# Performance work log

Hardware: AMD Instinct MI355X
Metric: run time of the kernel (lower is better)

## Reference

```python
import jax, jax.numpy as jnp
import numpy as np
from jax import lax

FH, FW, STRIDE = 100, 160, 16
IMG_H, IMG_W = FH * STRIDE, FW * STRIDE
A = 9
PRE_NMS, POST_NMS = 6000, 300  # prediction-path caps (training=0)
IOU_THR = 0.7
NEG = jnp.float32(-1e9)


def _make_anchor_map():
    # classic 3 scales x 3 aspect ratios, stride-16 grid, (y1,x1,y2,x2)
    scales = np.array([128.0, 256.0, 512.0], np.float32)
    ratios = np.array([0.5, 1.0, 2.0], np.float32)
    hs = (scales[:, None] * np.sqrt(ratios)[None, :]).reshape(-1)  # [9]
    ws = (scales[:, None] / np.sqrt(ratios)[None, :]).reshape(-1)
    cy = ((np.arange(FH, dtype=np.float32) + 0.5) * STRIDE)[:, None, None]
    cx = ((np.arange(FW, dtype=np.float32) + 0.5) * STRIDE)[None, :, None]
    y1 = np.broadcast_to(cy - 0.5 * hs, (FH, FW, A))
    x1 = np.broadcast_to(cx - 0.5 * ws, (FH, FW, A))
    y2 = np.broadcast_to(cy + 0.5 * hs, (FH, FW, A))
    x2 = np.broadcast_to(cx + 0.5 * ws, (FH, FW, A))
    am = np.stack([y1, x1, y2, x2], axis=-1)  # [FH,FW,9,4]
    return jnp.asarray(am.reshape(1, FH, FW, A * 4))


def setup_inputs() -> dict:
    key = jax.random.key(0)
    ks = jax.random.split(key, 6)
    return {
        "input_image": jax.random.uniform(ks[0], (1, IMG_H, IMG_W, 3), jnp.float32),
        "feature_map": jax.random.normal(ks[1], (1, FH, FW, 512), jnp.float32),
        "anchor_map": _make_anchor_map(),
        "anchor_valid_map": jnp.ones((1, FH, FW, A), jnp.float32),
        "W1": 0.01 * jax.random.normal(ks[2], (3, 3, 512, 512), jnp.float32),
        "b1": jnp.zeros((512,), jnp.float32),
        "Wc": 0.01 * jax.random.normal(ks[3], (1, 1, 512, A), jnp.float32),
        "bc": jnp.zeros((A,), jnp.float32),
        "Wr": 0.01 * jax.random.normal(ks[4], (1, 1, 512, 4 * A), jnp.float32),
        "br": jnp.zeros((4 * A,), jnp.float32),
        "training": 0,
    }


def _conv(x, w, b):
    return lax.conv_general_dilated(
        x, w, (1, 1), "SAME", dimension_numbers=("NHWC", "HWIO", "NHWC")
    ) + b


def _iou_one_vs_all(box, boxes):
    yy1 = jnp.maximum(box[0], boxes[:, 0])
    xx1 = jnp.maximum(box[1], boxes[:, 1])
    yy2 = jnp.minimum(box[2], boxes[:, 2])
    xx2 = jnp.minimum(box[3], boxes[:, 3])
    inter = jnp.maximum(yy2 - yy1, 0.0) * jnp.maximum(xx2 - xx1, 0.0)
    a1 = jnp.maximum(box[2] - box[0], 0.0) * jnp.maximum(box[3] - box[1], 0.0)
    a2 = jnp.maximum(boxes[:, 2] - boxes[:, 0], 0.0) * jnp.maximum(boxes[:, 3] - boxes[:, 1], 0.0)
    return inter / (a1 + a2 - inter + 1e-8)


def _nms(boxes, scores, max_out, iou_thr):
    # greedy NMS with fixed iteration count (padded with zero boxes)
    def step(s, _):
        i = jnp.argmax(s)
        best = s[i]
        box = boxes[i]
        valid = best > NEG * 0.5
        ious = _iou_one_vs_all(box, boxes)
        s = jnp.where(ious > iou_thr, NEG, s)
        s = s.at[i].set(NEG)
        out = jnp.where(valid, box, jnp.zeros_like(box))
        return s, out

    _, sel = lax.scan(step, scores, None, length=max_out)
    return sel  # [max_out, 4]


def reference(input_image, feature_map, anchor_map, anchor_valid_map,
              W1, b1, Wc, bc, Wr, br, training):
    pre_nms = 12000 if training else PRE_NMS
    post_nms = 2000 if training else POST_NMS
    # RPN head convs
    y = jax.nn.relu(_conv(feature_map, W1, b1))
    scores_map = jax.nn.sigmoid(_conv(y, Wc, bc))          # [1,FH,FW,9]
    reg_map = _conv(y, Wr, br)                              # [1,FH,FW,36]
    # flatten (extract_valid)
    anchors = anchor_map.reshape(-1, 4)                     # [N,4] (y1,x1,y2,x2)
    obj = scores_map.reshape(-1)                            # [N]
    deltas = reg_map.reshape(-1, 4)                         # [N,4] (ty,tx,th,tw)
    # delta -> bbox decode (means=0, stds=1)
    ah = anchors[:, 2] - anchors[:, 0]
    aw = anchors[:, 3] - anchors[:, 1]
    acy = anchors[:, 0] + 0.5 * ah
    acx = anchors[:, 1] + 0.5 * aw
    cy = acy + deltas[:, 0] * ah
    cx = acx + deltas[:, 1] * aw
    h = ah * jnp.exp(deltas[:, 2])
    w = aw * jnp.exp(deltas[:, 3])
    props = jnp.stack([cy - 0.5 * h, cx - 0.5 * w, cy + 0.5 * h, cx + 0.5 * w], axis=1)
    # sort desc by score, keep top pre_nms
    sc, idx = lax.top_k(obj, pre_nms)
    props = props[idx]
    # clip to image
    img_h = jnp.float32(input_image.shape[1])
    img_w = jnp.float32(input_image.shape[2])
    tl = jnp.maximum(props[:, 0:2], 0.0)
    y2 = jnp.minimum(props[:, 2], img_h)[:, None]
    x2 = jnp.minimum(props[:, 3], img_w)[:, None]
    props = jnp.concatenate([tl, y2, x2], axis=1)
    # min-size filter (>=16 on each side), via score masking (jit-safe)
    hh = props[:, 2] - props[:, 0]
    ww = props[:, 3] - props[:, 1]
    sc = jnp.where((hh >= 16.0) & (ww >= 16.0), sc, NEG)
    proposals = _nms(props, sc, post_nms, IOU_THR)          # [post_nms,4], zero-padded
    return scores_map, reg_map, proposals
```

## Files before the change

kernel.cpp:

```cpp
#include <hip/hip_runtime.h>
#include <math.h>

#define FHh 100
#define FWw 160
#define CIN 512
#define COUT 512
#define NPIX 16000
#define NANCH 144000
#define PRE_NMS 6000
#define POST_NMS 300
#define EQCAP 8192

#define BM 128
#define BN 128
#define BK 16
#define AST 130

typedef double d4 __attribute__((ext_vector_type(4)));

__device__ __forceinline__ unsigned fkey(float x){
  unsigned b = __float_as_uint(x);
  return (b & 0x80000000u) ? ~b : (b | 0x80000000u);
}
__device__ __forceinline__ unsigned long long dkey(double x){
  unsigned long long u = (unsigned long long)__double_as_longlong(x);
  return (u & 0x8000000000000000ull) ? ~u : (u | 0x8000000000000000ull);
}
__device__ __forceinline__ unsigned long long shfl_u64(unsigned long long x, int lane){
  unsigned lo = (unsigned)x, hi = (unsigned)(x >> 32);
  lo = __shfl(lo, lane, 64);
  hi = __shfl(hi, lane, 64);
  return ((unsigned long long)hi << 32) | lo;
}

__global__ __launch_bounds__(256) void prep_all(
    const float* __restrict__ fm, const float* __restrict__ Wc, const float* __restrict__ Wr,
    double* __restrict__ fmd, double* __restrict__ WcT, double* __restrict__ WrT)
{
  const int bid = blockIdx.x;
  if (bid < 8000){
    const int i = bid*256 + threadIdx.x;
    const float4 v = ((const float4*)fm)[i];
    double2* d = (double2*)(fmd + (size_t)i*4);
    d[0] = make_double2((double)v.x, (double)v.y);
    d[1] = make_double2((double)v.z, (double)v.w);
  } else {
    const int gid = (bid - 8000)*256 + threadIdx.x;
    if (gid < 45*512){
      const int n = gid >> 9, ci = gid & 511;
      if (n < 9) WcT[(size_t)n*512 + ci] = (double)Wc[ci*9 + n];
      else       WrT[(size_t)(n-9)*512 + ci] = (double)Wr[ci*36 + (n-9)];
    }
  }
}

__global__ __launch_bounds__(256, 2) void conv_gemm(
    const double* __restrict__ fmd, const float* __restrict__ W1,
    const float* __restrict__ b1, double* __restrict__ yd)
{
  __shared__ double As[BK * AST];
  __shared__ double Bs[BK * BN];
  const int bid  = blockIdx.x;
  const int cg   = bid / 125;
  const int tile = bid - cg*125;
  const int rp   = tile / 5;
  const int xseg = tile - rp*5;
  const int x0   = xseg*32;
  const int row0 = rp*4;
  const int co0  = cg*128;

  const int tid = threadIdx.x;
  const int lane = tid & 63;
  const int kl = lane >> 4;
  const int cl = lane & 15;
  const int wv = tid >> 6;
  const int wr = wv >> 1;
  const int wc = wv & 1;

  const int aoffA = kl*AST + wr*64 + cl;
  const int aoffB = kl*BN + wc*64 + cl;

  const int apx = tid >> 2;
  const int aks = (tid & 3) * 4;
  const int prA = apx >> 5;
  const int ac  = apx & 31;
  const int bkrow = tid >> 7;
  const int bcl   = tid & 127;

  d4 acc[4][4];
  #pragma unroll
  for (int mt = 0; mt < 4; ++mt)
    #pragma unroll
    for (int nt = 0; nt < 4; ++nt) acc[mt][nt] = (d4){0.0, 0.0, 0.0, 0.0};

  double pA0, pA1, pA2, pA3;
  double pB0, pB1, pB2, pB3;
  float pw[8];

  {
    const int grA = row0 + prA - 1;
    const int grB = grA + 2;
    const int gx  = x0 + ac - 1;
    if (grA >= 0 && gx >= 0){
      const double* p = fmd + ((size_t)(grA*FWw + gx))*CIN + aks;
      pA0 = p[0]; pA1 = p[1]; pA2 = p[2]; pA3 = p[3];
    } else { pA0 = pA1 = pA2 = pA3 = 0.0; }
    if (gx >= 0){
      const double* p = fmd + ((size_t)(grB*FWw + gx))*CIN + aks;
      pB0 = p[0]; pB1 = p[1]; pB2 = p[2]; pB3 = p[3];
    } else { pB0 = pB1 = pB2 = pB3 = 0.0; }
    const float* wb = W1 + (size_t)co0 + bcl;
    #pragma unroll
    for (int s = 0; s < 8; ++s) pw[s] = wb[(size_t)(2*s + bkrow)*512];
  }

  for (int ch = 0; ch < 288; ++ch){
    __syncthreads();
    As[(aks+0)*AST + apx] = pA0;
    As[(aks+1)*AST + apx] = pA1;
    As[(aks+2)*AST + apx] = pA2;
    As[(aks+3)*AST + apx] = pA3;
    As[(aks+0)*AST + apx + 64] = pB0;
    As[(aks+1)*AST + apx + 64] = pB1;
    As[(aks+2)*AST + apx + 64] = pB2;
    As[(aks+3)*AST + apx + 64] = pB3;
    #pragma unroll
    for (int s = 0; s < 8; ++s) Bs[s*256 + tid] = (double)pw[s];
    __syncthreads();
    const int nc = ch + 1;
    if (nc < 288){
      const int tap = nc >> 5;
      const int k0  = (nc & 31) * BK;
      const int dy = tap/3 - 1, dx = tap%3 - 1;
      const int grA = row0 + prA + dy;
      const int grB = grA + 2;
      const int gx  = x0 + ac + dx;
      const bool gxok = (gx >= 0 && gx < FWw);
      if (gxok && grA >= 0 && grA < FHh){
        const double* p = fmd + ((size_t)(grA*FWw + gx))*CIN + k0 + aks;
        pA0 = p[0]; pA1 = p[1]; pA2 = p[2]; pA3 = p[3];
      } else { pA0 = pA1 = pA2 = pA3 = 0.0; }
      if (gxok && grB >= 0 && grB < FHh){
        const double* p = fmd + ((size_t)(grB*FWw + gx))*CIN + k0 + aks;
        pB0 = p[0]; pB1 = p[1]; pB2 = p[2]; pB3 = p[3];
      } else { pB0 = pB1 = pB2 = pB3 = 0.0; }
      const float* wb = W1 + ((size_t)(tap*512 + k0 + bkrow))*512 + co0 + bcl;
      #pragma unroll
      for (int s = 0; s < 8; ++s) pw[s] = wb[(size_t)(2*s)*512];
    }
    #pragma unroll
    for (int k4 = 0; k4 < 4; ++k4){
      const double* Ap = As + k4*4*AST + aoffA;
      const double* Bp = Bs + k4*4*BN + aoffB;
      const double a0 = Ap[0], a1 = Ap[16], a2 = Ap[32], a3 = Ap[48];
      const double b0 = Bp[0], b1v = Bp[16], b2 = Bp[32], b3 = Bp[48];
      acc[0][0] = __builtin_amdgcn_mfma_f64_16x16x4f64(a0, b0,  acc[0][0], 0, 0, 0);
      acc[0][1] = __builtin_amdgcn_mfma_f64_16x16x4f64(a0, b1v, acc[0][1], 0, 0, 0);
      acc[0][2] = __builtin_amdgcn_mfma_f64_16x16x4f64(a0, b2,  acc[0][2], 0, 0, 0);
      acc[0][3] = __builtin_amdgcn_mfma_f64_16x16x4f64(a0, b3,  acc[0][3], 0, 0, 0);
      acc[1][0] = __builtin_amdgcn_mfma_f64_16x16x4f64(a1, b0,  acc[1][0], 0, 0, 0);
      acc[1][1] = __builtin_amdgcn_mfma_f64_16x16x4f64(a1, b1v, acc[1][1], 0, 0, 0);
      acc[1][2] = __builtin_amdgcn_mfma_f64_16x16x4f64(a1, b2,  acc[1][2], 0, 0, 0);
      acc[1][3] = __builtin_amdgcn_mfma_f64_16x16x4f64(a1, b3,  acc[1][3], 0, 0, 0);
      acc[2][0] = __builtin_amdgcn_mfma_f64_16x16x4f64(a2, b0,  acc[2][0], 0, 0, 0);
      acc[2][1] = __builtin_amdgcn_mfma_f64_16x16x4f64(a2, b1v, acc[2][1], 0, 0, 0);
      acc[2][2] = __builtin_amdgcn_mfma_f64_16x16x4f64(a2, b2,  acc[2][2], 0, 0, 0);
      acc[2][3] = __builtin_amdgcn_mfma_f64_16x16x4f64(a2, b3,  acc[2][3], 0, 0, 0);
      acc[3][0] = __builtin_amdgcn_mfma_f64_16x16x4f64(a3, b0,  acc[3][0], 0, 0, 0);
      acc[3][1] = __builtin_amdgcn_mfma_f64_16x16x4f64(a3, b1v, acc[3][1], 0, 0, 0);
      acc[3][2] = __builtin_amdgcn_mfma_f64_16x16x4f64(a3, b2,  acc[3][2], 0, 0, 0);
      acc[3][3] = __builtin_amdgcn_mfma_f64_16x16x4f64(a3, b3,  acc[3][3], 0, 0, 0);
    }
  }
  double bb[4];
  #pragma unroll
  for (int nt = 0; nt < 4; ++nt) bb[nt] = (double)b1[co0 + wc*64 + nt*16 + cl];
  #pragma unroll
  for (int mt = 0; mt < 4; ++mt){
    #pragma unroll
    for (int i = 0; i < 4; ++i){
      const int pxl = wr*64 + mt*16 + 4*i + kl;
      const int gpx = (row0 + (pxl >> 5))*FWw + x0 + (pxl & 31);
      double* yrow = yd + (size_t)gpx*CIN + co0 + wc*64 + cl;
      #pragma unroll
      for (int nt = 0; nt < 4; ++nt){
        yrow[nt*16] = fmax(acc[mt][nt][i] + bb[nt], 0.0);
      }
    }
  }
}

__global__ __launch_bounds__(256) void head2(
    const double* __restrict__ yd, const double* __restrict__ WcT, const float* __restrict__ bc,
    const double* __restrict__ WrT, const float* __restrict__ br,
    float* __restrict__ out, double* __restrict__ scored, double* __restrict__ regd)
{
  __shared__ double yl[8192];
  const int bid = blockIdx.x, t = threadIdx.x;
  const double2* src = (const double2*)(yd + (size_t)bid * 8192);
  double2* dst = (double2*)yl;
  for (int j = t; j < 4096; j += 256) dst[j] = src[j];
  __syncthreads();
  if (t < 180){
    const int n  = t % 45;
    const int pq = t / 45;
    const double* w = (n < 9) ? (WcT + (size_t)n*512) : (WrT + (size_t)(n-9)*512);
    const double* y0 = yl + (pq*4+0)*512;
    const double* y1 = yl + (pq*4+1)*512;
    const double* y2 = yl + (pq*4+2)*512;
    const double* y3 = yl + (pq*4+3)*512;
    double s0=0.0, s1=0.0, s2=0.0, s3=0.0;
    for (int ci = 0; ci < 512; ++ci){
      const double wv = w[ci];
      s0 = fma(y0[ci], wv, s0);
      s1 = fma(y1[ci], wv, s1);
      s2 = fma(y2[ci], wv, s2);
      s3 = fma(y3[ci], wv, s3);
    }
    const double sv[4] = {s0, s1, s2, s3};
    if (n < 9){
      const double bb = (double)bc[n];
      #pragma unroll
      for (int u = 0; u < 4; ++u){
        const double s = sv[u] + bb;
        const double sig = 1.0 / (1.0 + exp(-s));
        const int gi = (bid*16 + pq*4 + u)*9 + n;
        out[gi] = (float)sig;
        scored[gi] = sig;
      }
    } else {
      const int m = n - 9;
      const double bb = (double)br[m];
      #pragma unroll
      for (int u = 0; u < 4; ++u){
        const double s = sv[u] + bb;
        const int gi = (bid*16 + pq*4 + u)*36 + m;
        out[144000 + gi] = (float)s;
        regd[gi] = s;
      }
    }
  }
}

__global__ __launch_bounds__(256) void decode_hist(
    const float* __restrict__ amap, const double* __restrict__ scored,
    const double* __restrict__ regd, double* __restrict__ boxesd,
    unsigned* __restrict__ key32, unsigned long long* __restrict__ nmskey,
    unsigned* __restrict__ hist)
{
  const int i = blockIdx.x*256 + threadIdx.x;
  if (i >= NANCH) return;
  const double a0=(double)amap[4*i+0], a1=(double)amap[4*i+1];
  const double a2=(double)amap[4*i+2], a3=(double)amap[4*i+3];
  const double d0=regd[4*i+0], d1=regd[4*i+1], d2=regd[4*i+2], d3=regd[4*i+3];
  const double ah = a2 - a0, aw = a3 - a1;
  const double cy = a0 + 0.5*ah + d0*ah;
  const double cx = a1 + 0.5*aw + d1*aw;
  const double h = ah * exp(d2), w = aw * exp(d3);
  double y1 = cy - 0.5*h, x1 = cx - 0.5*w, y2 = cy + 0.5*h, x2 = cx + 0.5*w;
  y1 = fmax(y1, 0.0); x1 = fmax(x1, 0.0);
  y2 = fmin(y2, 1600.0); x2 = fmin(x2, 2560.0);
  boxesd[4*i+0]=y1; boxesd[4*i+1]=x1; boxesd[4*i+2]=y2; boxesd[4*i+3]=x2;
  const double obj = scored[i];
  const bool ok = (y2 - y1 >= 16.0) && (x2 - x1 >= 16.0);
  const unsigned k32 = fkey((float)obj);
  key32[i] = k32;
  nmskey[i] = ok ? dkey(obj) : dkey(-1e9);
  atomicAdd(&hist[k32 >> 16], 1u);
}

__global__ __launch_bounds__(1024) void scan_hi(const unsigned* __restrict__ hist, int* __restrict__ meta){
  __shared__ unsigned part[1024];
  const int t = threadIdx.x;
  unsigned s = 0;
  for (int j = 0; j < 64; ++j) s += hist[65535 - (t*64 + j)];
  part[t] = s;
  __syncthreads();
  for (int off = 1; off < 1024; off <<= 1){
    unsigned v = (t >= off) ? part[t - off] : 0u;
    __syncthreads();
    part[t] += v;
    __syncthreads();
  }
  const unsigned incl = part[t], excl = incl - s;
  if (excl < PRE_NMS && incl >= PRE_NMS){
    unsigned cum = excl;
    for (int j = 0; j < 64; ++j){
      const int bin = 65535 - (t*64 + j);
      const unsigned c = hist[bin];
      if (cum + c >= PRE_NMS){ meta[0] = bin; meta[1] = (int)cum; break; }
      cum += c;
    }
  }
}

__global__ __launch_bounds__(256) void hist_lo(const unsigned* __restrict__ key,
                                               const int* __restrict__ meta, unsigned* __restrict__ hist){
  const int i = blockIdx.x*256 + threadIdx.x;
  if (i < NANCH){
    const unsigned k = key[i];
    if ((int)(k >> 16) == meta[0]) atomicAdd(&hist[k & 0xFFFFu], 1u);
  }
}

__global__ __launch_bounds__(1024) void scan_lo(const unsigned* __restrict__ hist, int* __restrict__ meta){
  __shared__ unsigned part[1024];
  const int t = threadIdx.x;
  const unsigned G0 = (unsigned)meta[1];
  unsigned s = 0;
  for (int j = 0; j < 64; ++j) s += hist[65535 - (t*64 + j)];
  part[t] = s;
  __syncthreads();
  for (int off = 1; off < 1024; off <<= 1){
    unsigned v = (t >= off) ? part[t - off] : 0u;
    __syncthreads();
    part[t] += v;
    __syncthreads();
  }
  const unsigned incl = G0 + part[t], excl = incl - s;
  if (excl < PRE_NMS && incl >= PRE_NMS){
    unsigned cum = excl;
    for (int j = 0; j < 64; ++j){
      const int bin = 65535 - (t*64 + j);
      const unsigned c = hist[bin];
      if (cum + c >= PRE_NMS){
        meta[2] = (int)(((unsigned)meta[0] << 16) | (unsigned)bin);
        meta[3] = (int)cum;
        meta[4] = PRE_NMS - (int)cum;
        break;
      }
      cum += c;
    }
  }
}

__global__ __launch_bounds__(256) void compact_k(
    const unsigned* __restrict__ key, const unsigned long long* __restrict__ nmskey,
    const double* __restrict__ boxesd, const int* __restrict__ meta,
    int* __restrict__ cnt, double* __restrict__ selboxd,
    unsigned long long* __restrict__ selkey, int* __restrict__ eqidx)
{
  const int i = blockIdx.x*256 + threadIdx.x;
  if (i >= NANCH) return;
  const unsigned k = key[i];
  const unsigned T = (unsigned)meta[2];
  if (k > T){
    const int s = atomicAdd(&cnt[0], 1);
    selboxd[4*s+0]=boxesd[4*i+0]; selboxd[4*s+1]=boxesd[4*i+1];
    selboxd[4*s+2]=boxesd[4*i+2]; selboxd[4*s+3]=boxesd[4*i+3];
    selkey[s] = nmskey[i];
  } else if (k == T){
    const int e = atomicAdd(&cnt[1], 1);
    if (e < EQCAP) eqidx[e] = i;
  }
}

__global__ __launch_bounds__(256) void rankeq(
    const double* __restrict__ scored, const double* __restrict__ boxesd,
    const unsigned long long* __restrict__ nmskey,
    const int* __restrict__ meta, const int* __restrict__ cnt,
    const int* __restrict__ eqidx, double* __restrict__ selboxd,
    unsigned long long* __restrict__ selkey)
{
  __shared__ int eq[EQCAP];
  const int t = threadIdx.x;
  int E = cnt[1]; if (E > EQCAP) E = EQCAP;
  const int R = meta[4], G2 = meta[3];
  for (int j = t; j < E; j += 256) eq[j] = eqidx[j];
  __syncthreads();
  for (int j = t; j < E; j += 256){
    const int my = eq[j];
    const double smy = scored[my];
    int rank = 0;
    for (int k2 = 0; k2 < E; ++k2){
      const int ok = eq[k2];
      const double sk = scored[ok];
      rank += ((sk > smy) || (sk == smy && ok < my)) ? 1 : 0;
    }
    if (rank < R){
      const int s = G2 + rank;
      selboxd[4*s+0]=boxesd[4*my+0]; selboxd[4*s+1]=boxesd[4*my+1];
      selboxd[4*s+2]=boxesd[4*my+2]; selboxd[4*s+3]=boxesd[4*my+3];
      selkey[s] = nmskey[my];
    }
  }
}

__global__ __launch_bounds__(256) void rank_scatter(
    const unsigned long long* __restrict__ selkey, const double* __restrict__ selboxd,
    unsigned long long* __restrict__ skeys, double* __restrict__ sboxd)
{
  __shared__ unsigned long long k[PRE_NMS];
  const int t = threadIdx.x;
  for (int j = t; j < PRE_NMS; j += 256) k[j] = selkey[j];
  __syncthreads();
  const int j = blockIdx.x*256 + t;
  if (j >= PRE_NMS) return;
  const unsigned long long kj = k[j];
  int r = 0;
  for (int i = 0; i < PRE_NMS; i += 4){
    r += (int)((k[i+0] > kj) || (k[i+0] == kj && (i+0) < j));
    r += (int)((k[i+1] > kj) || (k[i+1] == kj && (i+1) < j));
    r += (int)((k[i+2] > kj) || (k[i+2] == kj && (i+2) < j));
    r += (int)((k[i+3] > kj) || (k[i+3] == kj && (i+3) < j));
  }
  skeys[r] = kj;
  sboxd[(size_t)r*4+0] = selboxd[(size_t)j*4+0];
  sboxd[(size_t)r*4+1] = selboxd[(size_t)j*4+1];
  sboxd[(size_t)r*4+2] = selboxd[(size_t)j*4+2];
  sboxd[(size_t)r*4+3] = selboxd[(size_t)j*4+3];
}

__global__ __launch_bounds__(256) void iou_bitmap(
    const double* __restrict__ sboxd, unsigned long long* __restrict__ rowbits)
{
  __shared__ double cbx[4096];
  const int g = blockIdx.y;
  const int r0 = blockIdx.x * 16;
  const int t = threadIdx.x;
  const int cbase = g * 1024;
  for (int e = t; e < 4096; e += 256){
    const int bi = cbase + (e >> 2);
    cbx[e] = (bi < PRE_NMS) ? sboxd[(size_t)bi*4 + (e & 3)] : 0.0;
  }
  __syncthreads();
  const int r = r0 + (t >> 4);
  const int w = t & 15;
  const double by1 = sboxd[(size_t)r*4+0], bx1 = sboxd[(size_t)r*4+1];
  const double by2 = sboxd[(size_t)r*4+2], bx2 = sboxd[(size_t)r*4+3];
  const double a1 = fmax(by2-by1, 0.0) * fmax(bx2-bx1, 0.0);
  unsigned long long bits = 0ull;
  for (int b = 0; b < 64; ++b){
    const int bcol = (b + w) & 63;
    const int j = cbase + w*64 + bcol;
    if (j < PRE_NMS){
      const int ce = (w*64 + bcol)*4;
      const double c0 = cbx[ce+0], c1 = cbx[ce+1], c2 = cbx[ce+2], c3 = cbx[ce+3];
      const double yy1 = fmax(by1, c0), xx1 = fmax(bx1, c1);
      const double yy2 = fmin(by2, c2), xx2 = fmin(bx2, c3);
      const double inter = fmax(yy2-yy1, 0.0) * fmax(xx2-xx1, 0.0);
      const double a2 = fmax(c2-c0, 0.0) * fmax(c3-c1, 0.0);
      const double iou = inter / (a1 + a2 - inter + 1e-8);
      if (iou > 0.7) bits |= (1ull << bcol);
    }
  }
  rowbits[(size_t)r*128 + g*16 + w] = bits;
}

__global__ __launch_bounds__(64) void greedy(
    const unsigned long long* __restrict__ skeys, const double* __restrict__ sboxd,
    const unsigned long long* __restrict__ rowbits, float* __restrict__ outp)
{
  const int t = threadIdx.x;
  const unsigned long long KEYTH = dkey(-5.0e8);
  int bad = PRE_NMS;
  for (int j = t; j < PRE_NMS; j += 64){
    if (skeys[j] <= KEYTH){ bad = j; break; }
  }
  #pragma unroll
  for (int off = 32; off > 0; off >>= 1){
    const int o = __shfl_down(bad, off, 64);
    bad = (o < bad) ? o : bad;
  }
  const int ilim = __builtin_amdgcn_readfirstlane(bad);

  unsigned long long s0 = 0ull, s1 = 0ull;
  int emitted = 0;
  for (int i = 0; i < ilim && emitted < POST_NMS; ++i){
    const int w = i >> 6, b = i & 63;
    const unsigned long long w0 = shfl_u64(s0, w & 63);
    const unsigned long long w1 = shfl_u64(s1, (w - 64) & 63);
    const unsigned long long word = (w < 64) ? w0 : w1;
    if (!((word >> b) & 1ull)){
      if (t < 4) outp[4*emitted + t] = (float)sboxd[(size_t)i*4 + t];
      s0 |= rowbits[(size_t)i*128 + t];
      if (t < 30) s1 |= rowbits[(size_t)i*128 + 64 + t];
      ++emitted;
    }
  }
  for (int r = emitted; r < POST_NMS; ++r)
    if (t < 4) outp[4*r + t] = 0.f;
}

extern "C" void kernel_launch(void* const* d_in, const int* in_sizes, int n_in,
                              void* d_out, int out_size, void* d_ws, size_t ws_size,
                              hipStream_t stream)
{
  const float* fm   = (const float*)d_in[1];
  const float* amap = (const float*)d_in[2];
  const float* W1   = (const float*)d_in[4];
  const float* b1   = (const float*)d_in[5];
  const float* Wc   = (const float*)d_in[6];
  const float* bc   = (const float*)d_in[7];
  const float* Wr   = (const float*)d_in[8];
  const float* br   = (const float*)d_in[9];
  float* out = (float*)d_out;

  char* base = (char*)d_ws;
  size_t off = 0;
  auto A = [&](size_t n) -> char* {
    char* p = base + off;
    off = (off + n + 255) & ~(size_t)255;
    return p;
  };
  double* yd      = (double*)A(65536000);
  double* fmd     = (double*)A(65536000);
  double* WcT     = (double*)A(36864);
  double* WrT     = (double*)A(147456);
  double* scored  = (double*)A(1152000);
  double* regd    = (double*)A(4608000);
  unsigned* histc = (unsigned*)A(524328);
  double* boxesd              = (double*)A(4608000);
  unsigned long long* nmskey  = (unsigned long long*)A(1152000);
  unsigned* key32             = (unsigned*)A(576000);
  double* selboxd             = (double*)A(192000);
  unsigned long long* selkey  = (unsigned long long*)A(48000);
  unsigned long long* skeys   = (unsigned long long*)A(48000);
  double* sboxd               = (double*)A(192000);
  unsigned long long* rowbits = (unsigned long long*)A(6144000);
  int* eqidx                  = (int*)A(32768);

  unsigned* hist1 = histc;
  unsigned* hist2 = histc + 65536;
  int* cnt        = (int*)(histc + 131072);
  int* meta       = cnt + 2;

  hipMemsetAsync(histc, 0, (size_t)524328, stream);

  hipLaunchKernelGGL(prep_all, dim3(8090), dim3(256), 0, stream,
                     fm, Wc, Wr, fmd, WcT, WrT);
  hipLaunchKernelGGL(conv_gemm, dim3(500), dim3(256), 0, stream, fmd, W1, b1, yd);
  hipLaunchKernelGGL(head2, dim3(1000), dim3(256), 0, stream, yd, WcT, bc, WrT, br, out, scored, regd);
  hipLaunchKernelGGL(decode_hist, dim3((NANCH + 255)/256), dim3(256), 0, stream,
                     amap, scored, regd, boxesd, key32, nmskey, hist1);
  hipLaunchKernelGGL(scan_hi, dim3(1), dim3(1024), 0, stream, hist1, meta);
  hipLaunchKernelGGL(hist_lo, dim3((NANCH + 255)/256), dim3(256), 0, stream, key32, meta, hist2);
  hipLaunchKernelGGL(scan_lo, dim3(1), dim3(1024), 0, stream, hist2, meta);
  hipLaunchKernelGGL(compact_k, dim3((NANCH + 255)/256), dim3(256), 0, stream,
                     key32, nmskey, boxesd, meta, cnt, selboxd, selkey, eqidx);
  hipLaunchKernelGGL(rankeq, dim3(1), dim3(256), 0, stream,
                     scored, boxesd, nmskey, meta, cnt, eqidx, selboxd, selkey);
  hipLaunchKernelGGL(rank_scatter, dim3((PRE_NMS + 255)/256), dim3(256), 0, stream,
                     selkey, selboxd, skeys, sboxd);
  hipLaunchKernelGGL(iou_bitmap, dim3(375, 6), dim3(256), 0, stream, sboxd, rowbits);
  hipLaunchKernelGGL(greedy, dim3(1), dim3(64), 0, stream, skeys, sboxd, rowbits, out + 720000);
}
```

Baseline: 2.096 ms.

## Reorder conv loop tap-inner with haloed input tile reused across taps and async weight loads

The 3x3 conv GEMM now loads a haloed 6x34 input tile per 16-channel chunk once and reuses it across all nine taps, instead of reloading shifted input for every tap. Weights are pre-converted to fp64 and streamed into double-buffered LDS with global_load_lds, while the feature map is read directly as fp32 and converted in-kernel, dropping the large fmd conversion pass. The aim is to cut global traffic for both the input and the prep kernel. The cost is extra syncs per tap and possible LDS bank conflicts from the strided halo indexing.

```diff
diff --git a/kernel.cpp b/kernel.cpp
--- a/kernel.cpp
+++ b/kernel.cpp
@@ -11,11 +11,6 @@
 #define POST_NMS 300
 #define EQCAP 8192
 
-#define BM 128
-#define BN 128
-#define BK 16
-#define AST 130
-
 typedef double d4 __attribute__((ext_vector_type(4)));
 
 __device__ __forceinline__ unsigned fkey(float x){
@@ -32,34 +27,38 @@
   hi = __shfl(hi, lane, 64);
   return ((unsigned long long)hi << 32) | lo;
 }
+__device__ __forceinline__ void gload_lds16(const void* g, void* l){
+  __builtin_amdgcn_global_load_lds(
+      (const __attribute__((address_space(1))) void*)g,
+      (__attribute__((address_space(3))) void*)l, 16, 0, 0);
+}
 
 __global__ __launch_bounds__(256) void prep_all(
-    const float* __restrict__ fm, const float* __restrict__ Wc, const float* __restrict__ Wr,
-    double* __restrict__ fmd, double* __restrict__ WcT, double* __restrict__ WrT)
+    const float* __restrict__ Wc, const float* __restrict__ Wr, const float* __restrict__ W1,
+    double* __restrict__ WcT, double* __restrict__ WrT, double* __restrict__ W64)
 {
   const int bid = blockIdx.x;
-  if (bid < 8000){
-    const int i = bid*256 + threadIdx.x;
-    const float4 v = ((const float4*)fm)[i];
-    double2* d = (double2*)(fmd + (size_t)i*4);
+  if (bid < 90){
+    const int gid = bid*256 + threadIdx.x;
+    const int n = gid >> 9, ci = gid & 511;
+    if (n < 9) WcT[(size_t)n*512 + ci] = (double)Wc[ci*9 + n];
+    else       WrT[(size_t)(n-9)*512 + ci] = (double)Wr[ci*36 + (n-9)];
+  } else {
+    const int i = (bid - 90)*256 + threadIdx.x;
+    const float4 v = ((const float4*)W1)[i];
+    double2* d = (double2*)(W64 + (size_t)i*4);
     d[0] = make_double2((double)v.x, (double)v.y);
     d[1] = make_double2((double)v.z, (double)v.w);
-  } else {
-    const int gid = (bid - 8000)*256 + threadIdx.x;
-    if (gid < 45*512){
-      const int n = gid >> 9, ci = gid & 511;
-      if (n < 9) WcT[(size_t)n*512 + ci] = (double)Wc[ci*9 + n];
-      else       WrT[(size_t)(n-9)*512 + ci] = (double)Wr[ci*36 + (n-9)];
-    }
   }
 }
 
 __global__ __launch_bounds__(256, 2) void conv_gemm(
-    const double* __restrict__ fmd, const float* __restrict__ W1,
+    const float* __restrict__ fm, const double* __restrict__ W64,
     const float* __restrict__ b1, double* __restrict__ yd)
 {
-  __shared__ double As[BK * AST];
-  __shared__ double Bs[BK * BN];
+  __shared__ double Ns[16*204];
+  __shared__ double Bsh[2][16*128];
+
   const int bid  = blockIdx.x;
   const int cg   = bid / 125;
   const int tile = bid - cg*125;
@@ -69,23 +68,55 @@
   const int row0 = rp*4;
   const int co0  = cg*128;
 
-  const int tid = threadIdx.x;
+  const int tid  = threadIdx.x;
   const int lane = tid & 63;
-  const int kl = lane >> 4;
-  const int cl = lane & 15;
-  const int wv = tid >> 6;
-  const int wr = wv >> 1;
-  const int wc = wv & 1;
-
-  const int aoffA = kl*AST + wr*64 + cl;
-  const int aoffB = kl*BN + wc*64 + cl;
-
-  const int apx = tid >> 2;
-  const int aks = (tid & 3) * 4;
-  const int prA = apx >> 5;
-  const int ac  = apx & 31;
-  const int bkrow = tid >> 7;
-  const int bcl   = tid & 127;
+  const int kl   = lane >> 4;
+  const int cl   = lane & 15;
+  const int wv   = tid >> 6;
+  const int wr   = wv >> 1;
+  const int wc   = wv & 1;
+
+  double pf[4][4];
+
+  auto APF_LOAD = [&](int kc){
+    #pragma unroll
+    for (int it = 0; it < 4; ++it){
+      const int t  = it*256 + tid;
+      const int px = t >> 2, kq = t & 3;
+      const int nr = px / 34, nc = px - nr*34;
+      const int row = row0 + nr - 1, col = x0 + nc - 1;
+      const bool ok = (t < 816) && (row >= 0) && (row < FHh) && (col >= 0) && (col < FWw);
+      if (ok){
+        const float4 v = *(const float4*)(fm + ((size_t)(row*FWw + col))*CIN + kc*16 + kq*4);
+        pf[it][0] = (double)v.x; pf[it][1] = (double)v.y;
+        pf[it][2] = (double)v.z; pf[it][3] = (double)v.w;
+      } else {
+        pf[it][0] = pf[it][1] = pf[it][2] = pf[it][3] = 0.0;
+      }
+    }
+  };
+  auto APF_WRITE = [&](){
+    #pragma unroll
+    for (int it = 0; it < 4; ++it){
+      const int t  = it*256 + tid;
+      const int px = t >> 2, kq = t & 3;
+      if (t < 816){
+        #pragma unroll
+        for (int u = 0; u < 4; ++u)
+          Ns[(kq*4 + u)*204 + px] = pf[it][u];
+      }
+    }
+  };
+  auto BGLDS = [&](int buf, int tap, int kc){
+    #pragma unroll
+    for (int s = 0; s < 4; ++s){
+      const int g    = s*256 + tid;
+      const int krow = g >> 6;
+      const int co2  = (g & 63)*2;
+      const double* src = W64 + ((size_t)(tap*512 + kc*16 + krow))*512 + co0 + co2;
+      gload_lds16(src, &Bsh[buf][krow*128 + co2]);
+    }
+  };
 
   d4 acc[4][4];
   #pragma unroll
@@ -93,83 +124,61 @@
     #pragma unroll
     for (int nt = 0; nt < 4; ++nt) acc[mt][nt] = (d4){0.0, 0.0, 0.0, 0.0};
 
-  double pA0, pA1, pA2, pA3;
-  double pB0, pB1, pB2, pB3;
-  float pw[8];
-
-  {
-    const int grA = row0 + prA - 1;
-    const int grB = grA + 2;
-    const int gx  = x0 + ac - 1;
-    if (grA >= 0 && gx >= 0){
-      const double* p = fmd + ((size_t)(grA*FWw + gx))*CIN + aks;
-      pA0 = p[0]; pA1 = p[1]; pA2 = p[2]; pA3 = p[3];
-    } else { pA0 = pA1 = pA2 = pA3 = 0.0; }
-    if (gx >= 0){
-      const double* p = fmd + ((size_t)(grB*FWw + gx))*CIN + aks;
-      pB0 = p[0]; pB1 = p[1]; pB2 = p[2]; pB3 = p[3];
-    } else { pB0 = pB1 = pB2 = pB3 = 0.0; }
-    const float* wb = W1 + (size_t)co0 + bcl;
-    #pragma unroll
-    for (int s = 0; s < 8; ++s) pw[s] = wb[(size_t)(2*s + bkrow)*512];
-  }
-
-  for (int ch = 0; ch < 288; ++ch){
-    __syncthreads();
-    As[(aks+0)*AST + apx] = pA0;
-    As[(aks+1)*AST + apx] = pA1;
-    As[(aks+2)*AST + apx] = pA2;
-    As[(aks+3)*AST + apx] = pA3;
-    As[(aks+0)*AST + apx + 64] = pB0;
-    As[(aks+1)*AST + apx + 64] = pB1;
-    As[(aks+2)*AST + apx + 64] = pB2;
-    As[(aks+3)*AST + apx + 64] = pB3;
-    #pragma unroll
-    for (int s = 0; s < 8; ++s) Bs[s*256 + tid] = (double)pw[s];
-    __syncthreads();
-    const int nc = ch + 1;
-    if (nc < 288){
-      const int tap = nc >> 5;
-      const int k0  = (nc & 31) * BK;
-      const int dy = tap/3 - 1, dx = tap%3 - 1;
-      const int grA = row0 + prA + dy;
-      const int grB = grA + 2;
-      const int gx  = x0 + ac + dx;
-      const bool gxok = (gx >= 0 && gx < FWw);
-      if (gxok && grA >= 0 && grA < FHh){
-        const double* p = fmd + ((size_t)(grA*FWw + gx))*CIN + k0 + aks;
-        pA0 = p[0]; pA1 = p[1]; pA2 = p[2]; pA3 = p[3];
-      } else { pA0 = pA1 = pA2 = pA3 = 0.0; }
-      if (gxok && grB >= 0 && grB < FHh){
-        const double* p = fmd + ((size_t)(grB*FWw + gx))*CIN + k0 + aks;
-        pB0 = p[0]; pB1 = p[1]; pB2 = p[2]; pB3 = p[3];
-      } else { pB0 = pB1 = pB2 = pB3 = 0.0; }
-      const float* wb = W1 + ((size_t)(tap*512 + k0 + bkrow))*512 + co0 + bcl;
+  APF_LOAD(0);
+  BGLDS(0, 0, 0);
+  APF_WRITE();
+  __syncthreads();
+
+  const int abase_t = kl*204 + cl;
+  const int bbase_t = kl*128 + wc*64 + cl;
+
+  for (int kc = 0; kc < 32; ++kc){
+    #pragma unroll 1
+    for (int tap = 0; tap < 9; ++tap){
+      const int ph  = kc*9 + tap;
+      const int cur = ph & 1;
+      if (ph + 1 < 288){
+        const int ntap = (tap == 8) ? 0 : tap + 1;
+        const int nkc  = (tap == 8) ? kc + 1 : kc;
+        BGLDS(cur ^ 1, ntap, nkc);
+      }
+      if (tap == 7 && kc < 31) APF_LOAD(kc + 1);
+      const int ty = tap / 3;
+      const int dy = ty - 1, dx = (tap - ty*3) - 1;
+      const double* An = Ns + abase_t + (wr*2 + dy + 1)*34 + (dx + 1);
+      const double* Bn = Bsh[cur] + bbase_t;
       #pragma unroll
-      for (int s = 0; s < 8; ++s) pw[s] = wb[(size_t)(2*s)*512];
-    }
-    #pragma unroll
-    for (int k4 = 0; k4 < 4; ++k4){
-      const double* Ap = As + k4*4*AST + aoffA;
-      const double* Bp = Bs + k4*4*BN + aoffB;
-      const double a0 = Ap[0], a1 = Ap[16], a2 = Ap[32], a3 = Ap[48];
-      const double b0 = Bp[0], b1v = Bp[16], b2 = Bp[32], b3 = Bp[48];
-      acc[0][0] = __builtin_amdgcn_mfma_f64_16x16x4f64(a0, b0,  acc[0][0], 0, 0, 0);
-      acc[0][1] = __builtin_amdgcn_mfma_f64_16x16x4f64(a0, b1v, acc[0][1], 0, 0, 0);
-      acc[0][2] = __builtin_amdgcn_mfma_f64_16x16x4f64(a0, b2,  acc[0][2], 0, 0, 0);
-      acc[0][3] = __builtin_amdgcn_mfma_f64_16x16x4f64(a0, b3,  acc[0][3], 0, 0, 0);
-      acc[1][0] = __builtin_amdgcn_mfma_f64_16x16x4f64(a1, b0,  acc[1][0], 0, 0, 0);
-      acc[1][1] = __builtin_amdgcn_mfma_f64_16x16x4f64(a1, b1v, acc[1][1], 0, 0, 0);
-      acc[1][2] = __builtin_amdgcn_mfma_f64_16x16x4f64(a1, b2,  acc[1][2], 0, 0, 0);
-      acc[1][3] = __builtin_amdgcn_mfma_f64_16x16x4f64(a1, b3,  acc[1][3], 0, 0, 0);
-      acc[2][0] = __builtin_amdgcn_mfma_f64_16x16x4f64(a2, b0,  acc[2][0], 0, 0, 0);
-      acc[2][1] = __builtin_amdgcn_mfma_f64_16x16x4f64(a2, b1v, acc[2][1], 0, 0, 0);
-      acc[2][2] = __builtin_amdgcn_mfma_f64_16x16x4f64(a2, b2,  acc[2][2], 0, 0, 0);
-      acc[2][3] = __builtin_amdgcn_mfma_f64_16x16x4f64(a2, b3,  acc[2][3], 0, 0, 0);
-      acc[3][0] = __builtin_amdgcn_mfma_f64_16x16x4f64(a3, b0,  acc[3][0], 0, 0, 0);
-      acc[3][1] = __builtin_amdgcn_mfma_f64_16x16x4f64(a3, b1v, acc[3][1], 0, 0, 0);
-      acc[3][2] = __builtin_amdgcn_mfma_f64_16x16x4f64(a3, b2,  acc[3][2], 0, 0, 0);
-      acc[3][3] = __builtin_amdgcn_mfma_f64_16x16x4f64(a3, b3,  acc[3][3], 0, 0, 0);
+      for (int k4 = 0; k4 < 4; ++k4){
+        const double a0 = An[k4*4*204 + 0*34 + 0];
+        const double a1 = An[k4*4*204 + 0*34 + 16];
+        const double a2 = An[k4*4*204 + 1*34 + 0];
+        const double a3 = An[k4*4*204 + 1*34 + 16];
+        const double b0 = Bn[k4*4*128 + 0];
+        const double b1v= Bn[k4*4*128 + 16];
+        const double b2 = Bn[k4*4*128 + 32];
+        const double b3 = Bn[k4*4*128 + 48];
+        acc[0][0] = __builtin_amdgcn_mfma_f64_16x16x4f64(a0, b0,  acc[0][0], 0, 0, 0);
+        acc[0][1] = __builtin_amdgcn_mfma_f64_16x16x4f64(a0, b1v, acc[0][1], 0, 0, 0);
+        acc[0][2] = __builtin_amdgcn_mfma_f64_16x16x4f64(a0, b2,  acc[0][2], 0, 0, 0);
+        acc[0][3] = __builtin_amdgcn_mfma_f64_16x16x4f64(a0, b3,  acc[0][3], 0, 0, 0);
+        acc[1][0] = __builtin_amdgcn_mfma_f64_16x16x4f64(a1, b0,  acc[1][0], 0, 0, 0);
+        acc[1][1] = __builtin_amdgcn_mfma_f64_16x16x4f64(a1, b1v, acc[1][1], 0, 0, 0);
+        acc[1][2] = __builtin_amdgcn_mfma_f64_16x16x4f64(a1, b2,  acc[1][2], 0, 0, 0);
+        acc[1][3] = __builtin_amdgcn_mfma_f64_16x16x4f64(a1, b3,  acc[1][3], 0, 0, 0);
+        acc[2][0] = __builtin_amdgcn_mfma_f64_16x16x4f64(a2, b0,  acc[2][0], 0, 0, 0);
+        acc[2][1] = __builtin_amdgcn_mfma_f64_16x16x4f64(a2, b1v, acc[2][1], 0, 0, 0);
+        acc[2][2] = __builtin_amdgcn_mfma_f64_16x16x4f64(a2, b2,  acc[2][2], 0, 0, 0);
+        acc[2][3] = __builtin_amdgcn_mfma_f64_16x16x4f64(a2, b3,  acc[2][3], 0, 0, 0);
+        acc[3][0] = __builtin_amdgcn_mfma_f64_16x16x4f64(a3, b0,  acc[3][0], 0, 0, 0);
+        acc[3][1] = __builtin_amdgcn_mfma_f64_16x16x4f64(a3, b1v, acc[3][1], 0, 0, 0);
+        acc[3][2] = __builtin_amdgcn_mfma_f64_16x16x4f64(a3, b2,  acc[3][2], 0, 0, 0);
+        acc[3][3] = __builtin_amdgcn_mfma_f64_16x16x4f64(a3, b3,  acc[3][3], 0, 0, 0);
+      }
+      __syncthreads();
+      if (tap == 8 && kc < 31){
+        APF_WRITE();
+        __syncthreads();
+      }
     }
   }
   double bb[4];
@@ -504,7 +513,7 @@
     return p;
   };
   double* yd      = (double*)A(65536000);
-  double* fmd     = (double*)A(65536000);
+  double* W64     = (double*)A(18874368);
   double* WcT     = (double*)A(36864);
   double* WrT     = (double*)A(147456);
   double* scored  = (double*)A(1152000);
@@ -527,9 +536,9 @@
 
   hipMemsetAsync(histc, 0, (size_t)524328, stream);
 
-  hipLaunchKernelGGL(prep_all, dim3(8090), dim3(256), 0, stream,
-                     fm, Wc, Wr, fmd, WcT, WrT);
-  hipLaunchKernelGGL(conv_gemm, dim3(500), dim3(256), 0, stream, fmd, W1, b1, yd);
+  hipLaunchKernelGGL(prep_all, dim3(2394), dim3(256), 0, stream,
+                     Wc, Wr, W1, WcT, WrT, W64);
+  hipLaunchKernelGGL(conv_gemm, dim3(500), dim3(256), 0, stream, fm, W64, b1, yd);
   hipLaunchKernelGGL(head2, dim3(1000), dim3(256), 0, stream, yd, WcT, bc, WrT, br, out, scored, regd);
   hipLaunchKernelGGL(decode_hist, dim3((NANCH + 255)/256), dim3(256), 0, stream,
                      amap, scored, regd, boxesd, key32, nmskey, hist1);
```

Measured after the change: 2.059 ms. About the same (-1.8%).
